# Optimization experiments

Hardware: AMD Instinct MI355X
Metric: run time of the kernel (lower is better)

Reference implementation:

```python
import jax, jax.numpy as jnp
from jax import lax
import numpy as np

K_SIZE = 3  # deformable kernel size
PAD = 1
STRIDE = 1


def _conv3x3(x, w, b):
    # plain 3x3 conv, pad 1, stride 1, NCHW/OIHW
    y = lax.conv_general_dilated(x, w, window_strides=(1, 1),
                                 padding=[(1, 1), (1, 1)],
                                 dimension_numbers=('NCHW', 'OIHW', 'NCHW'))
    return y + b[None, :, None, None]


def _deform_sample(x, py, px):
    """Bilinear sample x [B,C,H,W] at float coords py,px [B,K,Ho,Wo].
    Out-of-bounds samples contribute zero (matches torchvision deform_conv2d).
    Returns [B,C,K,Ho,Wo]."""
    B, C, H, W = x.shape
    y0 = jnp.floor(py)
    x0 = jnp.floor(px)
    gat = jax.vmap(lambda img, iy, ix: img[:, iy, ix])  # per-batch gather -> [C,K,Ho,Wo]
    out = jnp.zeros((B, C) + py.shape[1:], dtype=x.dtype)
    for yc, xc in ((y0, x0), (y0, x0 + 1), (y0 + 1, x0), (y0 + 1, x0 + 1)):
        wgt = (1.0 - jnp.abs(py - yc)) * (1.0 - jnp.abs(px - xc))
        valid = (yc >= 0) & (yc <= H - 1) & (xc >= 0) & (xc <= W - 1)
        wgt = jnp.where(valid, wgt, 0.0)
        iy = jnp.clip(yc, 0, H - 1).astype(jnp.int32)
        ix = jnp.clip(xc, 0, W - 1).astype(jnp.int32)
        out = out + wgt[:, None] * gat(x, iy, ix)
    return out


def reference(x, w_off, b_off, w_mask, b_mask, w_dcn, b_dcn):
    k = K_SIZE
    K = k * k
    B, C, H, W = x.shape
    # offset conv (2*K channels: (dy, dx) pairs per kernel position, row-major)
    offset = _conv3x3(x, w_off, b_off)            # [B, 2K, H, W]
    mask = jax.nn.sigmoid(_conv3x3(x, w_mask, b_mask))  # [B, K, H, W]
    off = offset.reshape(B, K, 2, H, W)
    dy, dx = off[:, :, 0], off[:, :, 1]
    ki = (jnp.arange(K) // k).astype(x.dtype)  # kernel row index
    kj = (jnp.arange(K) % k).astype(x.dtype)   # kernel col index
    # sampling coordinates: out position * stride - pad + kernel pos + learned offset
    py = (jnp.arange(H, dtype=x.dtype)[None, None, :, None] * STRIDE - PAD
          + ki[None, :, None, None] + dy)
    px = (jnp.arange(W, dtype=x.dtype)[None, None, None, :] * STRIDE - PAD
          + kj[None, :, None, None] + dx)
    val = _deform_sample(x, py, px) * mask[:, None]   # [B,C,K,H,W]
    Cout = w_dcn.shape[0]
    out = jnp.einsum('ock,bckhw->bohw', w_dcn.reshape(Cout, C, K), val)
    return out + b_dcn[None, :, None, None]


def setup_inputs() -> dict:
    key = jax.random.key(0)
    ks = jax.random.split(key, 6)
    B, C, Cout, H, W, k = 4, 256, 256, 64, 64, 3
    K = k * k
    x = jax.random.normal(ks[0], (B, C, H, W), dtype=jnp.float32)
    # NOTE: original inits offset/mask conv to zeros (degenerate -> plain conv).
    # Use small random weights so offsets/masks are nontrivial but local.
    w_off = jax.random.normal(ks[1], (2 * K, C, 3, 3), dtype=jnp.float32) * 0.01
    b_off = jnp.zeros((2 * K,), dtype=jnp.float32)
    w_mask = jax.random.normal(ks[2], (K, C, 3, 3), dtype=jnp.float32) * 0.01
    b_mask = jnp.zeros((K,), dtype=jnp.float32)
    fan_in = C * K
    w_dcn = jax.random.normal(ks[3], (Cout, C, 3, 3), dtype=jnp.float32) / np.sqrt(fan_in)
    b_dcn = jnp.zeros((Cout,), dtype=jnp.float32)
    return {"x": x, "w_off": w_off, "b_off": b_off, "w_mask": w_mask,
            "b_mask": b_mask, "w_dcn": w_dcn, "b_dcn": b_dcn}
```

## Files before the change

### kernel.cpp

```cpp
#include <hip/hip_runtime.h>
#include <math.h>

#define B_ 4
#define C_ 256
#define CO_ 256
#define H_ 64
#define W_ 64
#define HW_ 4096
#define KK_ 9
#define NCH_ 27

typedef __attribute__((ext_vector_type(8))) short bf16x8;
typedef __attribute__((ext_vector_type(4))) float f32x4;
typedef __attribute__((ext_vector_type(2))) float f32x2;

__device__ inline unsigned short f32_to_bf16(float f) {
    unsigned int u = __float_as_uint(f);
    unsigned int r = (u + 0x7FFFu + ((u >> 16) & 1u)) >> 16;
    return (unsigned short)r;
}

__global__ void prep_all(const float* __restrict__ x, unsigned short* __restrict__ xTh,
                         const float* __restrict__ w_dcn, const float* __restrict__ w_off,
                         const float* __restrict__ w_mask,
                         unsigned short* __restrict__ wTs, unsigned short* __restrict__ wCs) {
    __shared__ float tile[32][33];
    __shared__ float lw[2304];
    const int t = threadIdx.x;
    const int bid = blockIdx.x;
    if (bid < 4096) {
        const int b = bid >> 10;
        const int rem = bid & 1023;
        const int c0 = (rem >> 7) << 5;
        const int hw0 = (rem & 127) << 5;
        const float* xb = x + ((size_t)b << 20);
        unsigned short* xTb = xTh + ((size_t)b << 20);
        {
            int r = t >> 3, q = t & 7;
            float4 v = *(const float4*)(xb + ((size_t)(c0 + r) << 12) + hw0 + (q << 2));
            tile[r][(q << 2) + 0] = v.x;
            tile[r][(q << 2) + 1] = v.y;
            tile[r][(q << 2) + 2] = v.z;
            tile[r][(q << 2) + 3] = v.w;
        }
        __syncthreads();
        {
            int hw = t >> 3, c4 = t & 7;
            ushort4 o;
            o.x = f32_to_bf16(tile[(c4 << 2) + 0][hw]);
            o.y = f32_to_bf16(tile[(c4 << 2) + 1][hw]);
            o.z = f32_to_bf16(tile[(c4 << 2) + 2][hw]);
            o.w = f32_to_bf16(tile[(c4 << 2) + 3][hw]);
            *(ushort4*)(xTb + ((size_t)(hw0 + hw) << 8) + c0 + (c4 << 2)) = o;
        }
    } else if (bid < 4352) {
        const int o = bid - 4096;
        for (int e = t; e < 576; e += 256)
            ((float4*)lw)[e] = ((const float4*)(w_dcn + (size_t)o * 2304))[e];
        __syncthreads();
        for (int e = t; e < 2304; e += 256) {
            int k = e >> 8, c = e & 255;
            int chunk = (k << 2) + (c >> 6), ck = c & 63;
            int pos = (o << 6) + (((ck >> 3) ^ (o & 7)) << 3) + (ck & 7);
            wTs[(size_t)chunk * 16384 + pos] = f32_to_bf16(lw[c * 9 + k]);
        }
    } else {
        const int ch = bid - 4352;
        const float* src = (ch < 18) ? w_off + (size_t)ch * 2304
                         : (ch < NCH_) ? w_mask + (size_t)(ch - 18) * 2304
                         : nullptr;
        if (src) {
            for (int e = t; e < 576; e += 256) ((float4*)lw)[e] = ((const float4*)src)[e];
        } else {
            for (int e = t; e < 2304; e += 256) lw[e] = 0.f;
        }
        __syncthreads();
        for (int e = t; e < 2304; e += 256) {
            int k = e >> 8, c = e & 255;
            int chunk = (k << 2) + (c >> 6), ck = c & 63;
            int pos = (ch << 6) + (((ck >> 3) ^ (ch & 7)) << 3) + (ck & 7);
            wCs[(size_t)chunk * 2048 + pos] = f32_to_bf16(lw[c * 9 + k]);
        }
    }
}

__global__ __launch_bounds__(256, 2) void conv_mfma(
    const unsigned short* __restrict__ xTh, const unsigned short* __restrict__ wCs,
    const float* __restrict__ b_off, const float* __restrict__ b_mask,
    float* __restrict__ offmask) {
    __shared__ alignas(16) unsigned short wlds[3][2048];
    __shared__ alignas(16) unsigned short xlds[3][2048];
    const int t = threadIdx.x;
    const int bid = blockIdx.x;
    const int b = (bid & 7) >> 1;
    const int ph = bid & 1;
    const int hh = bid >> 3;
    const unsigned short* xb = xTh + ((size_t)b << 20);

    auto stage_w = [&](int chunk, int slot) {
        const unsigned short* g = wCs + ((size_t)chunk << 11) + (t << 3);
        __builtin_amdgcn_global_load_lds(
            (const __attribute__((address_space(1))) unsigned int*)g,
            (__attribute__((address_space(3))) unsigned int*)&wlds[slot][t << 3], 16, 0, 0);
    };

    const int xp = t >> 3, xcs = t & 7;
    uint4 xr;
    bool xvalid;
    auto xload = [&](int chunk) {
        int k = chunk >> 2, cc = chunk & 3;
        int ki = k / 3, kj = k % 3;
        int py = hh + ki - 1;
        int px = (ph << 5) + xp + kj - 1;
        xvalid = (py >= 0) & (py < H_) & (px >= 0) & (px < W_);
        int pyc = min(max(py, 0), 63), pxc = min(max(px, 0), 63);
        xr = *(const uint4*)(xb + (((size_t)((pyc << 6) + pxc)) << 8) + (cc << 6) + (xcs << 3));
    };
    auto xwrite = [&](int slot) {
        uint4 u = xvalid ? xr : make_uint4(0u, 0u, 0u, 0u);
        *(uint4*)&xlds[slot][(xp << 6) + ((xcs ^ (xp & 7)) << 3)] = u;
    };

    const int wid = t >> 6, lane = t & 63;
    const int wc = wid >> 1, wp = wid & 1;
    const int m16 = lane & 15, kg = lane >> 4;
    f32x4 acc = {};

    auto compute = [&](int slot) {
#pragma unroll
        for (int ks = 0; ks < 2; ++ks) {
            int s = (ks << 2) + kg;
            int o = (wc << 4) + m16;
            bf16x8 a = *(const bf16x8*)&wlds[slot][(o << 6) + ((s ^ (o & 7)) << 3)];
            int p = (wp << 4) + m16;
            bf16x8 bf = *(const bf16x8*)&xlds[slot][(p << 6) + ((s ^ (p & 7)) << 3)];
            acc = __builtin_amdgcn_mfma_f32_16x16x32_bf16(a, bf, acc, 0, 0, 0);
        }
    };

    xload(0);
    stage_w(0, 0);
    asm volatile("s_waitcnt vmcnt(1)" ::: "memory");
    xwrite(0);

    for (int c = 0; c < 35; ++c) {
        xload(c + 1);
        stage_w(c + 1, (c + 1) % 3);
        asm volatile("s_waitcnt vmcnt(1)" ::: "memory");
        xwrite((c + 1) % 3);
        asm volatile("s_waitcnt lgkmcnt(0)" ::: "memory");
        __builtin_amdgcn_s_barrier();
        asm volatile("" ::: "memory");
        compute(c % 3);
    }
    asm volatile("s_waitcnt vmcnt(0)" ::: "memory");
    asm volatile("s_waitcnt lgkmcnt(0)" ::: "memory");
    __builtin_amdgcn_s_barrier();
    asm volatile("" ::: "memory");
    compute(35 % 3);

    const int pix = (hh << 6) + (ph << 5) + (wp << 4) + m16;
#pragma unroll
    for (int r = 0; r < 4; ++r) {
        int ch = (wc << 4) + (kg << 2) + r;
        if (ch < NCH_) {
            float bias = (ch < 18) ? b_off[ch] : b_mask[ch - 18];
            offmask[(((size_t)b * NCH_ + ch) << 12) + pix] = acc[r] + bias;
        }
    }
}

__global__ __launch_bounds__(512, 4) void dcn_fused(
    const unsigned short* __restrict__ xTh, const float* __restrict__ offmask,
    const unsigned short* __restrict__ wTs, unsigned short* __restrict__ part) {
    __shared__ ushort4 cwh[576];
    __shared__ uchar4 coffb[576];
    __shared__ alignas(16) unsigned short wbuf[2][16384];
    __shared__ alignas(16) unsigned short vbuf[4096];

    const int t = threadIdx.x;
    const int bid = blockIdx.x;
    const int b = (bid & 7) >> 1;
    const int half = bid & 1;
    const int tile64 = bid >> 3;
    const int pix0 = tile64 << 6;
    const unsigned short* xb = xTh + ((size_t)b << 20);
    const float* omb = offmask + (((size_t)b * NCH_) << 12);

    for (int e = t; e < 576; e += 512) {
        int k = e >> 6, p = e & 63;
        int pix = pix0 + p;
        int hh = pix >> 6, ww = pix & 63;
        float dy = omb[((size_t)(2 * k) << 12) + pix];
        float dx = omb[((size_t)(2 * k + 1) << 12) + pix];
        float ml = omb[((size_t)(18 + k) << 12) + pix];
        float m = 1.f / (1.f + __expf(-ml));
        float py = (float)(hh - 1 + (k / 3)) + dy;
        float px = (float)(ww - 1 + (k % 3)) + dx;
        float fy0 = floorf(py), fx0 = floorf(px);
        float ay = py - fy0, ax = px - fx0;
        bool y0v = (fy0 >= 0.f) && (fy0 <= 63.f);
        bool y1v = (fy0 >= -1.f) && (fy0 <= 62.f);
        bool x0v = (fx0 >= 0.f) && (fx0 <= 63.f);
        bool x1v = (fx0 >= -1.f) && (fx0 <= 62.f);
        int y0 = (int)fy0, x0 = (int)fx0;
        int iy0 = min(max(y0, 0), 63), iy1 = min(max(y0 + 1, 0), 63);
        int ix0 = min(max(x0, 0), 63), ix1 = min(max(x0 + 1, 0), 63);
        float w00 = (y0v && x0v) ? m * (1.f - ay) * (1.f - ax) : 0.f;
        float w01 = (y0v && x1v) ? m * (1.f - ay) * ax : 0.f;
        float w10 = (y1v && x0v) ? m * ay * (1.f - ax) : 0.f;
        float w11 = (y1v && x1v) ? m * ay * ax : 0.f;
        cwh[e] = make_ushort4(f32_to_bf16(w00), f32_to_bf16(w01),
                              f32_to_bf16(w10), f32_to_bf16(w11));
        coffb[e] = make_uchar4((unsigned char)iy0, (unsigned char)ix0,
                               (unsigned char)iy1, (unsigned char)ix1);
    }

    const int oct = t & 7, pq = t >> 3;
    const int wid = t >> 6, lane = t & 63;
    const int wo = wid >> 1, wp = wid & 1;
    const int m16 = lane & 15, kg = lane >> 4;
    const int vslot = (pq << 6) + ((oct ^ (pq & 7)) << 3);

    auto stage_w = [&](int c, int slot) {
        int gc = ((c >> 1) << 2) + (half << 1) + (c & 1);
#pragma unroll
        for (int r = 0; r < 4; ++r) {
            int off16 = (r << 9) + t;
            const unsigned short* g = wTs + ((size_t)gc << 14) + (off16 << 3);
            __builtin_amdgcn_global_load_lds(
                (const __attribute__((address_space(1))) unsigned int*)g,
                (__attribute__((address_space(3))) unsigned int*)&wbuf[slot][off16 << 3], 16, 0, 0);
        }
    };

    auto gather = [&](int c, uint4* g) {
        int k = c >> 1, cc = (half << 1) + (c & 1);
        uchar4 q = coffb[(k << 6) + pq];
        const unsigned short* cb = xb + (cc << 6) + (oct << 3);
        g[0] = *(const uint4*)(cb + ((((int)q.x << 6) + q.y) << 8));
        g[1] = *(const uint4*)(cb + ((((int)q.x << 6) + q.w) << 8));
        g[2] = *(const uint4*)(cb + ((((int)q.z << 6) + q.y) << 8));
        g[3] = *(const uint4*)(cb + ((((int)q.z << 6) + q.w) << 8));
    };

    auto finish = [&](int c, const uint4* g) {
        int k = c >> 1;
        ushort4 wv = cwh[(k << 6) + pq];
        float w0 = __uint_as_float((unsigned int)wv.x << 16);
        float w1 = __uint_as_float((unsigned int)wv.y << 16);
        float w2 = __uint_as_float((unsigned int)wv.z << 16);
        float w3 = __uint_as_float((unsigned int)wv.w << 16);
        union { uint4 v; unsigned int u[4]; } A, B2, C2, D2;
        A.v = g[0]; B2.v = g[1]; C2.v = g[2]; D2.v = g[3];
        unsigned int o4[4];
#pragma unroll
        for (int j = 0; j < 4; ++j) {
            f32x2 a2 = {__uint_as_float(A.u[j] << 16),  __uint_as_float(A.u[j] & 0xffff0000u)};
            f32x2 b2 = {__uint_as_float(B2.u[j] << 16), __uint_as_float(B2.u[j] & 0xffff0000u)};
            f32x2 c2 = {__uint_as_float(C2.u[j] << 16), __uint_as_float(C2.u[j] & 0xffff0000u)};
            f32x2 d2 = {__uint_as_float(D2.u[j] << 16), __uint_as_float(D2.u[j] & 0xffff0000u)};
            f32x2 v2 = a2 * w0 + b2 * w1 + c2 * w2 + d2 * w3;
            unsigned int pk;
            asm("v_cvt_pk_bf16_f32 %0, %1, %2" : "=v"(pk) : "v"(v2.x), "v"(v2.y));
            o4[j] = pk;
        }
        *(uint4*)&vbuf[vslot] = make_uint4(o4[0], o4[1], o4[2], o4[3]);
    };

    f32x4 acc[4][2] = {};

    auto compute = [&](int slot) {
#pragma unroll
        for (int ks = 0; ks < 2; ++ks) {
            int s = (ks << 2) + kg;
            bf16x8 aF[4], bF[2];
#pragma unroll
            for (int i = 0; i < 4; ++i) {
                int o = (wo << 6) + (i << 4) + m16;
                aF[i] = *(const bf16x8*)&wbuf[slot][(o << 6) + ((s ^ (o & 7)) << 3)];
            }
#pragma unroll
            for (int j = 0; j < 2; ++j) {
                int p = (wp << 5) + (j << 4) + m16;
                bF[j] = *(const bf16x8*)&vbuf[(p << 6) + ((s ^ (p & 7)) << 3)];
            }
#pragma unroll
            for (int i = 0; i < 4; ++i)
#pragma unroll
                for (int j = 0; j < 2; ++j)
                    acc[i][j] = __builtin_amdgcn_mfma_f32_16x16x32_bf16(
                        aF[i], bF[j], acc[i][j], 0, 0, 0);
        }
    };

    uint4 gA[4], gB[4];

    __syncthreads();
    gather(0, gA);
    stage_w(0, 0);

#define HALFSTEP(CUR, GCUR, GNXT, NW1, NW2)                              \
    __builtin_amdgcn_s_barrier();                                        \
    asm volatile("" ::: "memory");                                       \
    if ((CUR) + 1 < 18) { gather((CUR) + 1, GNXT); stage_w((CUR) + 1, ((CUR) + 1) & 1); } \
    asm volatile("s_waitcnt vmcnt(" #NW1 ")" ::: "memory");              \
    finish((CUR), GCUR);                                                 \
    asm volatile("s_waitcnt vmcnt(" #NW2 ") lgkmcnt(0)" ::: "memory");   \
    __builtin_amdgcn_s_barrier();                                        \
    asm volatile("" ::: "memory");                                       \
    __builtin_amdgcn_s_setprio(1);                                       \
    compute((CUR) & 1);                                                  \
    __builtin_amdgcn_s_setprio(0);

    for (int c = 0; c < 16; c += 2) {
        HALFSTEP(c, gA, gB, 12, 8)
        HALFSTEP(c + 1, gB, gA, 12, 8)
    }
    HALFSTEP(16, gA, gB, 12, 8)
    HALFSTEP(17, gB, gA, 4, 0)
#undef HALFSTEP

    unsigned short* pd = part + (((size_t)((half << 2) + b)) << 20);
#pragma unroll
    for (int i = 0; i < 4; ++i) {
        int ob = (wo << 6) + (i << 4) + (kg << 2);
#pragma unroll
        for (int j = 0; j < 2; ++j) {
            int p = pix0 + (wp << 5) + (j << 4) + m16;
#pragma unroll
            for (int r = 0; r < 4; ++r) {
                int oo = ob + r;
                pd[(((size_t)oo) << 12) + p] = f32_to_bf16(acc[i][j][r]);
            }
        }
    }
}

__global__ __launch_bounds__(256) void combine_out(
    const unsigned short* __restrict__ part, const float* __restrict__ b_dcn,
    float* __restrict__ out) {
    int i = (blockIdx.x * 256 + threadIdx.x) << 3;
    float bias = b_dcn[(i >> 12) & 255];
    union { uint4 v; unsigned int u[4]; } A, B2;
    A.v  = *(const uint4*)(part + i);
    B2.v = *(const uint4*)(part + ((size_t)4 << 20) + i);
    float r[8];
#pragma unroll
    for (int j = 0; j < 4; ++j) {
        float a_lo = __uint_as_float(A.u[j] << 16);
        float a_hi = __uint_as_float(A.u[j] & 0xffff0000u);
        float b_lo = __uint_as_float(B2.u[j] << 16);
        float b_hi = __uint_as_float(B2.u[j] & 0xffff0000u);
        r[2 * j]     = a_lo + b_lo + bias;
        r[2 * j + 1] = a_hi + b_hi + bias;
    }
    *(float4*)(out + i)     = make_float4(r[0], r[1], r[2], r[3]);
    *(float4*)(out + i + 4) = make_float4(r[4], r[5], r[6], r[7]);
}

extern "C" void kernel_launch(void* const* d_in, const int* in_sizes, int n_in,
                              void* d_out, int out_size, void* d_ws, size_t ws_size,
                              hipStream_t stream) {
    const float* x      = (const float*)d_in[0];
    const float* w_off  = (const float*)d_in[1];
    const float* b_off  = (const float*)d_in[2];
    const float* w_mask = (const float*)d_in[3];
    const float* b_mask = (const float*)d_in[4];
    const float* w_dcn  = (const float*)d_in[5];
    const float* b_dcn  = (const float*)d_in[6];
    float* out = (float*)d_out;

    float* ws = (float*)d_ws;
    float* offmask = ws;
    unsigned short* xTh = (unsigned short*)(offmask + (size_t)B_ * NCH_ * HW_);
    unsigned short* wTs = xTh + ((size_t)B_ * HW_ * C_);
    unsigned short* wCs = wTs + (size_t)36 * 16384;
    unsigned short* part = wCs + (size_t)36 * 2048;

    prep_all<<<dim3(4384), dim3(256), 0, stream>>>(x, xTh, w_dcn, w_off, w_mask, wTs, wCs);
    conv_mfma<<<dim3(512), dim3(256), 0, stream>>>(xTh, wCs, b_off, b_mask, offmask);
    dcn_fused<<<dim3(512), dim3(512), 0, stream>>>(xTh, offmask, wTs, part);
    combine_out<<<dim3(2048), dim3(256), 0, stream>>>(part, b_dcn, out);
}
```

Baseline: 71.71 us.

## Double-buffer sample tile, drop a barrier per step, deepen offset conv chunks

In dcn_fused the bilinear coefficients and indices now live in per-thread registers instead of shared memory, and the initial syncthreads is removed. The sampled-value tile is double-buffered, so each half-step needs only one barrier, and the weight staging for the next step is issued after that barrier. The offset/mask conv processes two K-chunks per barrier, doubling its LDS buffers and halving its barrier count. The trade-off is higher register and LDS pressure, which could lower occupancy, plus a wait-count schedule that has to be right for correctness.

```diff
diff --git a/kernel.cpp b/kernel.cpp
--- a/kernel.cpp
+++ b/kernel.cpp
@@ -88,37 +88,40 @@
     const unsigned short* __restrict__ xTh, const unsigned short* __restrict__ wCs,
     const float* __restrict__ b_off, const float* __restrict__ b_mask,
     float* __restrict__ offmask) {
-    __shared__ alignas(16) unsigned short wlds[3][2048];
-    __shared__ alignas(16) unsigned short xlds[3][2048];
+    __shared__ alignas(16) unsigned short wlds[3][4096];
+    __shared__ alignas(16) unsigned short xlds[3][4096];
     const int t = threadIdx.x;
     const int bid = blockIdx.x;
     const int b = (bid & 7) >> 1;
-    const int ph = bid & 1;
+    const int ph2 = bid & 1;
     const int hh = bid >> 3;
     const unsigned short* xb = xTh + ((size_t)b << 20);
 
-    auto stage_w = [&](int chunk, int slot) {
-        const unsigned short* g = wCs + ((size_t)chunk << 11) + (t << 3);
-        __builtin_amdgcn_global_load_lds(
-            (const __attribute__((address_space(1))) unsigned int*)g,
-            (__attribute__((address_space(3))) unsigned int*)&wlds[slot][t << 3], 16, 0, 0);
+    auto stage_w2 = [&](int phase, int slot) {
+#pragma unroll
+        for (int sub = 0; sub < 2; ++sub) {
+            int chunk = (phase << 1) + sub;
+            const unsigned short* g = wCs + ((size_t)chunk << 11) + (t << 3);
+            __builtin_amdgcn_global_load_lds(
+                (const __attribute__((address_space(1))) unsigned int*)g,
+                (__attribute__((address_space(3))) unsigned int*)&wlds[slot][(sub << 11) + (t << 3)],
+                16, 0, 0);
+        }
     };
 
     const int xp = t >> 3, xcs = t & 7;
-    uint4 xr;
-    bool xvalid;
-    auto xload = [&](int chunk) {
+    auto xload1 = [&](int chunk, uint4& xr, bool& xv) {
         int k = chunk >> 2, cc = chunk & 3;
         int ki = k / 3, kj = k % 3;
         int py = hh + ki - 1;
-        int px = (ph << 5) + xp + kj - 1;
-        xvalid = (py >= 0) & (py < H_) & (px >= 0) & (px < W_);
+        int px = (ph2 << 5) + xp + kj - 1;
+        xv = (py >= 0) & (py < H_) & (px >= 0) & (px < W_);
         int pyc = min(max(py, 0), 63), pxc = min(max(px, 0), 63);
         xr = *(const uint4*)(xb + (((size_t)((pyc << 6) + pxc)) << 8) + (cc << 6) + (xcs << 3));
     };
-    auto xwrite = [&](int slot) {
-        uint4 u = xvalid ? xr : make_uint4(0u, 0u, 0u, 0u);
-        *(uint4*)&xlds[slot][(xp << 6) + ((xcs ^ (xp & 7)) << 3)] = u;
+    auto xwrite1 = [&](int slot, int sub, const uint4& xr, bool xv) {
+        uint4 u = xv ? xr : make_uint4(0u, 0u, 0u, 0u);
+        *(uint4*)&xlds[slot][(sub << 11) + (xp << 6) + ((xcs ^ (xp & 7)) << 3)] = u;
     };
 
     const int wid = t >> 6, lane = t & 63;
@@ -126,40 +129,49 @@
     const int m16 = lane & 15, kg = lane >> 4;
     f32x4 acc = {};
 
-    auto compute = [&](int slot) {
-#pragma unroll
-        for (int ks = 0; ks < 2; ++ks) {
-            int s = (ks << 2) + kg;
-            int o = (wc << 4) + m16;
-            bf16x8 a = *(const bf16x8*)&wlds[slot][(o << 6) + ((s ^ (o & 7)) << 3)];
-            int p = (wp << 4) + m16;
-            bf16x8 bf = *(const bf16x8*)&xlds[slot][(p << 6) + ((s ^ (p & 7)) << 3)];
-            acc = __builtin_amdgcn_mfma_f32_16x16x32_bf16(a, bf, acc, 0, 0, 0);
-        }
-    };
-
-    xload(0);
-    stage_w(0, 0);
-    asm volatile("s_waitcnt vmcnt(1)" ::: "memory");
-    xwrite(0);
-
-    for (int c = 0; c < 35; ++c) {
-        xload(c + 1);
-        stage_w(c + 1, (c + 1) % 3);
-        asm volatile("s_waitcnt vmcnt(1)" ::: "memory");
-        xwrite((c + 1) % 3);
+    auto compute2 = [&](int slot) {
+#pragma unroll
+        for (int sub = 0; sub < 2; ++sub)
+#pragma unroll
+            for (int ks = 0; ks < 2; ++ks) {
+                int s = (ks << 2) + kg;
+                int o = (wc << 4) + m16;
+                bf16x8 a = *(const bf16x8*)&wlds[slot][(sub << 11) + (o << 6) + ((s ^ (o & 7)) << 3)];
+                int p = (wp << 4) + m16;
+                bf16x8 bf = *(const bf16x8*)&xlds[slot][(sub << 11) + (p << 6) + ((s ^ (p & 7)) << 3)];
+                acc = __builtin_amdgcn_mfma_f32_16x16x32_bf16(a, bf, acc, 0, 0, 0);
+            }
+    };
+
+    uint4 xr0, xr1;
+    bool xv0, xv1;
+
+    xload1(0, xr0, xv0);
+    xload1(1, xr1, xv1);
+    stage_w2(0, 0);
+    asm volatile("s_waitcnt vmcnt(2)" ::: "memory");
+    xwrite1(0, 0, xr0, xv0);
+    xwrite1(0, 1, xr1, xv1);
+
+    for (int ph = 0; ph < 17; ++ph) {
+        xload1((ph << 1) + 2, xr0, xv0);
+        xload1((ph << 1) + 3, xr1, xv1);
+        stage_w2(ph + 1, (ph + 1) % 3);
+        asm volatile("s_waitcnt vmcnt(2)" ::: "memory");
+        xwrite1((ph + 1) % 3, 0, xr0, xv0);
+        xwrite1((ph + 1) % 3, 1, xr1, xv1);
         asm volatile("s_waitcnt lgkmcnt(0)" ::: "memory");
         __builtin_amdgcn_s_barrier();
         asm volatile("" ::: "memory");
-        compute(c % 3);
+        compute2(ph % 3);
     }
     asm volatile("s_waitcnt vmcnt(0)" ::: "memory");
     asm volatile("s_waitcnt lgkmcnt(0)" ::: "memory");
     __builtin_amdgcn_s_barrier();
     asm volatile("" ::: "memory");
-    compute(35 % 3);
-
-    const int pix = (hh << 6) + (ph << 5) + (wp << 4) + m16;
+    compute2(17 % 3);
+
+    const int pix = (hh << 6) + (ph2 << 5) + (wp << 4) + m16;
 #pragma unroll
     for (int r = 0; r < 4; ++r) {
         int ch = (wc << 4) + (kg << 2) + r;
@@ -173,10 +185,8 @@
 __global__ __launch_bounds__(512, 4) void dcn_fused(
     const unsigned short* __restrict__ xTh, const float* __restrict__ offmask,
     const unsigned short* __restrict__ wTs, unsigned short* __restrict__ part) {
-    __shared__ ushort4 cwh[576];
-    __shared__ uchar4 coffb[576];
     __shared__ alignas(16) unsigned short wbuf[2][16384];
-    __shared__ alignas(16) unsigned short vbuf[4096];
+    __shared__ alignas(16) unsigned short vbuf[2][4096];
 
     const int t = threadIdx.x;
     const int bid = blockIdx.x;
@@ -187,40 +197,44 @@
     const unsigned short* xb = xTh + ((size_t)b << 20);
     const float* omb = offmask + (((size_t)b * NCH_) << 12);
 
-    for (int e = t; e < 576; e += 512) {
-        int k = e >> 6, p = e & 63;
-        int pix = pix0 + p;
-        int hh = pix >> 6, ww = pix & 63;
-        float dy = omb[((size_t)(2 * k) << 12) + pix];
-        float dx = omb[((size_t)(2 * k + 1) << 12) + pix];
-        float ml = omb[((size_t)(18 + k) << 12) + pix];
-        float m = 1.f / (1.f + __expf(-ml));
-        float py = (float)(hh - 1 + (k / 3)) + dy;
-        float px = (float)(ww - 1 + (k % 3)) + dx;
-        float fy0 = floorf(py), fx0 = floorf(px);
-        float ay = py - fy0, ax = px - fx0;
-        bool y0v = (fy0 >= 0.f) && (fy0 <= 63.f);
-        bool y1v = (fy0 >= -1.f) && (fy0 <= 62.f);
-        bool x0v = (fx0 >= 0.f) && (fx0 <= 63.f);
-        bool x1v = (fx0 >= -1.f) && (fx0 <= 62.f);
-        int y0 = (int)fy0, x0 = (int)fx0;
-        int iy0 = min(max(y0, 0), 63), iy1 = min(max(y0 + 1, 0), 63);
-        int ix0 = min(max(x0, 0), 63), ix1 = min(max(x0 + 1, 0), 63);
-        float w00 = (y0v && x0v) ? m * (1.f - ay) * (1.f - ax) : 0.f;
-        float w01 = (y0v && x1v) ? m * (1.f - ay) * ax : 0.f;
-        float w10 = (y1v && x0v) ? m * ay * (1.f - ax) : 0.f;
-        float w11 = (y1v && x1v) ? m * ay * ax : 0.f;
-        cwh[e] = make_ushort4(f32_to_bf16(w00), f32_to_bf16(w01),
-                              f32_to_bf16(w10), f32_to_bf16(w11));
-        coffb[e] = make_uchar4((unsigned char)iy0, (unsigned char)ix0,
-                               (unsigned char)iy1, (unsigned char)ix1);
-    }
-
     const int oct = t & 7, pq = t >> 3;
     const int wid = t >> 6, lane = t & 63;
     const int wo = wid >> 1, wp = wid & 1;
     const int m16 = lane & 15, kg = lane >> 4;
     const int vslot = (pq << 6) + ((oct ^ (pq & 7)) << 3);
+
+    ushort4 cwhR[9];
+    uchar4 coffR[9];
+    {
+        const int pixq = pix0 + pq;
+        const int hhq = pixq >> 6, wwq = pixq & 63;
+#pragma unroll
+        for (int k = 0; k < 9; ++k) {
+            float dy = omb[((size_t)(2 * k) << 12) + pixq];
+            float dx = omb[((size_t)(2 * k + 1) << 12) + pixq];
+            float ml = omb[((size_t)(18 + k) << 12) + pixq];
+            float m = 1.f / (1.f + __expf(-ml));
+            float py = (float)(hhq - 1 + (k / 3)) + dy;
+            float px = (float)(wwq - 1 + (k % 3)) + dx;
+            float fy0 = floorf(py), fx0 = floorf(px);
+            float ay = py - fy0, ax = px - fx0;
+            bool y0v = (fy0 >= 0.f) && (fy0 <= 63.f);
+            bool y1v = (fy0 >= -1.f) && (fy0 <= 62.f);
+            bool x0v = (fx0 >= 0.f) && (fx0 <= 63.f);
+            bool x1v = (fx0 >= -1.f) && (fx0 <= 62.f);
+            int y0 = (int)fy0, x0 = (int)fx0;
+            int iy0 = min(max(y0, 0), 63), iy1 = min(max(y0 + 1, 0), 63);
+            int ix0 = min(max(x0, 0), 63), ix1 = min(max(x0 + 1, 0), 63);
+            float w00 = (y0v && x0v) ? m * (1.f - ay) * (1.f - ax) : 0.f;
+            float w01 = (y0v && x1v) ? m * (1.f - ay) * ax : 0.f;
+            float w10 = (y1v && x0v) ? m * ay * (1.f - ax) : 0.f;
+            float w11 = (y1v && x1v) ? m * ay * ax : 0.f;
+            cwhR[k] = make_ushort4(f32_to_bf16(w00), f32_to_bf16(w01),
+                                   f32_to_bf16(w10), f32_to_bf16(w11));
+            coffR[k] = make_uchar4((unsigned char)iy0, (unsigned char)ix0,
+                                   (unsigned char)iy1, (unsigned char)ix1);
+        }
+    }
 
     auto stage_w = [&](int c, int slot) {
         int gc = ((c >> 1) << 2) + (half << 1) + (c & 1);
@@ -236,7 +250,7 @@
 
     auto gather = [&](int c, uint4* g) {
         int k = c >> 1, cc = (half << 1) + (c & 1);
-        uchar4 q = coffb[(k << 6) + pq];
+        uchar4 q = coffR[k];
         const unsigned short* cb = xb + (cc << 6) + (oct << 3);
         g[0] = *(const uint4*)(cb + ((((int)q.x << 6) + q.y) << 8));
         g[1] = *(const uint4*)(cb + ((((int)q.x << 6) + q.w) << 8));
@@ -246,7 +260,7 @@
 
     auto finish = [&](int c, const uint4* g) {
         int k = c >> 1;
-        ushort4 wv = cwh[(k << 6) + pq];
+        ushort4 wv = cwhR[k];
         float w0 = __uint_as_float((unsigned int)wv.x << 16);
         float w1 = __uint_as_float((unsigned int)wv.y << 16);
         float w2 = __uint_as_float((unsigned int)wv.z << 16);
@@ -265,7 +279,7 @@
             asm("v_cvt_pk_bf16_f32 %0, %1, %2" : "=v"(pk) : "v"(v2.x), "v"(v2.y));
             o4[j] = pk;
         }
-        *(uint4*)&vbuf[vslot] = make_uint4(o4[0], o4[1], o4[2], o4[3]);
+        *(uint4*)&vbuf[c & 1][vslot] = make_uint4(o4[0], o4[1], o4[2], o4[3]);
     };
 
     f32x4 acc[4][2] = {};
@@ -283,7 +297,7 @@
 #pragma unroll
             for (int j = 0; j < 2; ++j) {
                 int p = (wp << 5) + (j << 4) + m16;
-                bF[j] = *(const bf16x8*)&vbuf[(p << 6) + ((s ^ (p & 7)) << 3)];
+                bF[j] = *(const bf16x8*)&vbuf[slot][(p << 6) + ((s ^ (p & 7)) << 3)];
             }
 #pragma unroll
             for (int i = 0; i < 4; ++i)
@@ -296,28 +310,26 @@
 
     uint4 gA[4], gB[4];
 
-    __syncthreads();
     gather(0, gA);
     stage_w(0, 0);
 
-#define HALFSTEP(CUR, GCUR, GNXT, NW1, NW2)                              \
+#define HALFSTEP(CUR, GCUR, GNXT, NWA, NWB)                              \
+    if ((CUR) + 1 < 18) gather((CUR) + 1, GNXT);                         \
+    asm volatile("s_waitcnt vmcnt(" #NWA ")" ::: "memory");              \
+    finish((CUR), GCUR);                                                 \
+    asm volatile("s_waitcnt vmcnt(" #NWB ") lgkmcnt(0)" ::: "memory");   \
     __builtin_amdgcn_s_barrier();                                        \
     asm volatile("" ::: "memory");                                       \
-    if ((CUR) + 1 < 18) { gather((CUR) + 1, GNXT); stage_w((CUR) + 1, ((CUR) + 1) & 1); } \
-    asm volatile("s_waitcnt vmcnt(" #NW1 ")" ::: "memory");              \
-    finish((CUR), GCUR);                                                 \
-    asm volatile("s_waitcnt vmcnt(" #NW2 ") lgkmcnt(0)" ::: "memory");   \
-    __builtin_amdgcn_s_barrier();                                        \
-    asm volatile("" ::: "memory");                                       \
+    if ((CUR) + 1 < 18) stage_w((CUR) + 1, ((CUR) + 1) & 1);             \
     __builtin_amdgcn_s_setprio(1);                                       \
     compute((CUR) & 1);                                                  \
     __builtin_amdgcn_s_setprio(0);
 
     for (int c = 0; c < 16; c += 2) {
-        HALFSTEP(c, gA, gB, 12, 8)
-        HALFSTEP(c + 1, gB, gA, 12, 8)
-    }
-    HALFSTEP(16, gA, gB, 12, 8)
+        HALFSTEP(c, gA, gB, 8, 4)
+        HALFSTEP(c + 1, gB, gA, 8, 4)
+    }
+    HALFSTEP(16, gA, gB, 8, 4)
     HALFSTEP(17, gB, gA, 4, 0)
 #undef HALFSTEP
 
```

After: 75.59 us. +5.4%, slower.
